# Kernel tuning notes

Measured on AMD Instinct MI355X. Metric: run time of the kernel, lower is better.

Reference implementation:

```python
import jax, jax.numpy as jnp
import numpy as np

B, D = 16384, 1024
H1, H2 = 512, 256
T = 3          # num_tasks
E_SH = 2       # num_shared_experts
E_SP = 2       # num_specific_experts
G = E_SH + E_SP


def setup_inputs() -> dict:
    key = jax.random.key(0)
    ks = jax.random.split(key, 8)
    def glorot(k, shape, fan_in, fan_out):
        return jax.random.normal(k, shape, jnp.float32) * jnp.sqrt(2.0 / (fan_in + fan_out))
    return {
        "x": jax.random.normal(ks[0], (B, D), jnp.float32),
        "shared_W1": glorot(ks[1], (E_SH, D, H1), D, H1),
        "shared_b1": jnp.zeros((E_SH, H1), jnp.float32),
        "shared_W2": glorot(ks[2], (E_SH, H1, H2), H1, H2),
        "shared_b2": jnp.zeros((E_SH, H2), jnp.float32),
        "spec_W1": glorot(ks[3], (T, E_SP, D, H1), D, H1),
        "spec_b1": jnp.zeros((T, E_SP, H1), jnp.float32),
        "spec_W2": glorot(ks[4], (T, E_SP, H1, H2), H1, H2),
        "spec_b2": jnp.zeros((T, E_SP, H2), jnp.float32),
        "gate_W": glorot(ks[5], (T, D, G), D, G),
        "gate_b": jnp.zeros((T, G), jnp.float32),
    }


def reference(x, shared_W1, shared_b1, shared_W2, shared_b2,
              spec_W1, spec_b1, spec_W2, spec_b2, gate_W, gate_b):
    # Shared experts: two-layer MLP with relu, batched over experts. [B, E_SH, H2]
    sh = jax.nn.relu(jnp.einsum('bi,eih->beh', x, shared_W1) + shared_b1)
    sh = jax.nn.relu(jnp.einsum('beh,eho->beo', sh, shared_W2) + shared_b2)
    # Task-specific experts, batched over (task, expert). [B, T, E_SP, H2]
    sp = jax.nn.relu(jnp.einsum('bi,teih->bteh', x, spec_W1) + spec_b1)
    sp = jax.nn.relu(jnp.einsum('bteh,teho->bteo', sp, spec_W2) + spec_b2)
    # Gates: single linear layer per task + softmax over G=E_SH+E_SP experts. [B, T, G]
    gate = jax.nn.softmax(jnp.einsum('bi,tig->btg', x, gate_W) + gate_b, axis=-1)
    # Experts stacked in order: shared first, then specific (matches tf.stack order).
    sh_b = jnp.broadcast_to(sh[:, None], (B, T, E_SH, H2))
    experts = jnp.concatenate([sh_b, sp], axis=2)  # [B, T, G, H2]
    # Gate-weighted sum over the expert axis -> per-task outputs [B, T, H2]
    out = jnp.einsum('btgh,btg->bth', experts, gate)
    return out
```

## Files before the change

### kernel.cpp

```cpp
#include <hip/hip_runtime.h>
#include <hip/hip_bf16.h>
#include <stdint.h>

#define B_SZ 16384
#define D_SZ 1024
#define H1_SZ 512
#define H2_SZ 256
#define T_SZ 3
#define ESH 2
#define NE 8

typedef __bf16 bf16x8 __attribute__((ext_vector_type(8)));
typedef float f32x4 __attribute__((ext_vector_type(4)));
typedef unsigned short u16;
typedef u16 u16x8 __attribute__((ext_vector_type(8)));

__device__ __forceinline__ u16 f2bf(float f) {
  union { float f; uint32_t u; } v; v.f = f;
  uint32_t u = v.u;
  uint32_t r = (u + 0x7FFFu + ((u >> 16) & 1u)) >> 16;
  return (u16)r;
}
__device__ __forceinline__ float bf2f(u16 b) {
  union { uint32_t u; float f; } v; v.u = ((uint32_t)b) << 16;
  return v.f;
}

__device__ __forceinline__ void gload16(const u16* src, u16* dst_lds) {
  __builtin_amdgcn_global_load_lds(
      (const __attribute__((address_space(1))) void*)src,
      (__attribute__((address_space(3))) void*)dst_lds, 16, 0, 0);
}

__global__ __launch_bounds__(256) void cast_f32_to_bf16(
    const float* __restrict__ in, u16* __restrict__ out, int n8) {
  int i = blockIdx.x * blockDim.x + threadIdx.x;
  if (i >= n8) return;
  const float4* p = (const float4*)in + (size_t)i * 2;
  float4 a = p[0], b = p[1];
  u16x8 o;
  o[0] = f2bf(a.x); o[1] = f2bf(a.y); o[2] = f2bf(a.z); o[3] = f2bf(a.w);
  o[4] = f2bf(b.x); o[5] = f2bf(b.y); o[6] = f2bf(b.z); o[7] = f2bf(b.w);
  *((u16x8*)out + i) = o;
}

__global__ __launch_bounds__(256) void transpose_cast(
    const float* __restrict__ src, u16* __restrict__ dst, int K, int N) {
  __shared__ float tile[32][33];
  size_t e = blockIdx.z;
  const float* s = src + e * (size_t)K * N;
  u16* d = dst + e * (size_t)K * N;
  int n0 = blockIdx.x * 32, k0 = blockIdx.y * 32;
  int tx = threadIdx.x, ty = threadIdx.y;
#pragma unroll
  for (int i = ty; i < 32; i += 8)
    tile[i][tx] = s[(size_t)(k0 + i) * N + n0 + tx];
  __syncthreads();
#pragma unroll
  for (int i = ty; i < 32; i += 8)
    d[(size_t)(n0 + i) * K + k0 + tx] = f2bf(tile[tx][i]);
}

__global__ __launch_bounds__(512, 2) void gemm_ring(
    const u16* __restrict__ A, size_t strideAe,
    const u16* __restrict__ Bt,
    const float* __restrict__ bias_sh, const float* __restrict__ bias_sp,
    u16* __restrict__ C, int M, int N, int K, int ntn) {
  __shared__ __align__(16) u16 lds[4 * 16384];
  const int tid = threadIdx.x;
  const int wid = tid >> 6, lane = tid & 63;
  const int fr = lane & 15, fq = lane >> 4;
  const int wr = wid >> 2, wc = wid & 3;

  const int nwg = gridDim.x;
  const int bid = blockIdx.x;
  const int l = (bid & 7) * (nwg >> 3) + (bid >> 3);
  const int e = l & 7;
  const int rest = l >> 3;
  const int ntile = rest % ntn;
  const int mtile = rest / ntn;
  const int m0 = mtile * 256, n0 = ntile * 256;

  const u16* Ae = A + (size_t)e * strideAe;
  const u16* Be = Bt + (size_t)e * (size_t)N * K;
  const int NT = K >> 5;

  const int c0 = tid, c1 = 512 + tid;
  const int ar0 = c0 >> 2, as0 = (c0 & 3) ^ ((ar0 >> 1) & 3);
  const int ar1 = c1 >> 2, as1 = (c1 & 3) ^ ((ar1 >> 1) & 3);
  const u16* pA0 = Ae + (size_t)(m0 + ar0) * K + as0 * 8;
  const u16* pA1 = Ae + (size_t)(m0 + ar1) * K + as1 * 8;
  const u16* pB0 = Be + (size_t)(n0 + ar0) * K + as0 * 8;
  const u16* pB1 = Be + (size_t)(n0 + ar1) * K + as1 * 8;
  const int dst0 = (wid * 64) * 8;
  const int dst1 = (512 + wid * 64) * 8;

  int offA[8], offB[4];
#pragma unroll
  for (int m = 0; m < 8; ++m) {
    int r = wr * 128 + m * 16 + fr;
    offA[m] = r * 32 + ((fq ^ ((r >> 1) & 3)) * 8);
  }
#pragma unroll
  for (int n = 0; n < 4; ++n) {
    int cg = wc * 64 + n * 16 + fr;
    offB[n] = 8192 + cg * 32 + ((fq ^ ((cg >> 1) & 3)) * 8);
  }

  f32x4 acc[8][4] = {};

#define STAGE(t) do { const int sbs = ((t) & 3) * 16384;              \
    gload16(pA0 + (t) * 32, &lds[sbs + dst0]);                        \
    gload16(pA1 + (t) * 32, &lds[sbs + dst1]);                        \
    gload16(pB0 + (t) * 32, &lds[sbs + 8192 + dst0]);                 \
    gload16(pB1 + (t) * 32, &lds[sbs + 8192 + dst1]); } while (0)

  STAGE(0); STAGE(1); STAGE(2);
  asm volatile("s_waitcnt vmcnt(8)");
  __builtin_amdgcn_s_barrier();
  __builtin_amdgcn_sched_barrier(0);

  for (int t = 0; t < NT; ++t) {
    const u16* sl = &lds[(t & 3) * 16384];
    bf16x8 av[8], bv[4];
#pragma unroll
    for (int m = 0; m < 8; ++m) av[m] = *(const bf16x8*)&sl[offA[m]];
#pragma unroll
    for (int n = 0; n < 4; ++n) bv[n] = *(const bf16x8*)&sl[offB[n]];
    if (t + 3 < NT) STAGE(t + 3);
    __builtin_amdgcn_s_setprio(1);
#pragma unroll
    for (int m = 0; m < 8; ++m)
#pragma unroll
      for (int n = 0; n < 4; ++n)
        acc[m][n] = __builtin_amdgcn_mfma_f32_16x16x32_bf16(av[m], bv[n], acc[m][n], 0, 0, 0);
    __builtin_amdgcn_s_setprio(0);
    asm volatile("s_waitcnt vmcnt(8)");
    __builtin_amdgcn_s_barrier();
    __builtin_amdgcn_sched_barrier(0);
  }
#undef STAGE

  const float* bias = (e < ESH) ? (bias_sh + (size_t)e * N)
                                : (bias_sp + (size_t)(e - ESH) * N);
  u16* Ce = C + (size_t)e * (size_t)M * N;
  float bb[4];
#pragma unroll
  for (int n = 0; n < 4; ++n) bb[n] = bias[n0 + wc * 64 + n * 16 + fr];

  const int src = (tid >> 5);
  const int cc = (tid & 31) * 8;
#pragma unroll
  for (int half = 0; half < 2; ++half) {
    if (wr == half) {
#pragma unroll
      for (int m = 0; m < 8; ++m) {
#pragma unroll
        for (int n = 0; n < 4; ++n) {
          const int col = wc * 64 + n * 16 + fr;
          f32x4 a = acc[m][n];
#pragma unroll
          for (int r = 0; r < 4; ++r) {
            float v = a[r] + bb[n];
            v = v > 0.f ? v : 0.f;
            lds[(m * 16 + fq * 4 + r) * 256 + col] = f2bf(v);
          }
        }
      }
    }
    __builtin_amdgcn_s_barrier();
#pragma unroll
    for (int pass = 0; pass < 8; ++pass) {
      const int lr = pass * 16 + src;
      const int gr = m0 + half * 128 + lr;
      u16x8 vv = *(const u16x8*)&lds[lr * 256 + cc];
      *(u16x8*)&Ce[(size_t)gr * N + n0 + cc] = vv;
    }
    __builtin_amdgcn_s_barrier();
  }
}

__global__ __launch_bounds__(256) void gates_kernel(
    const float* __restrict__ x, const float* __restrict__ gW,
    const float* __restrict__ gb, float* __restrict__ gates) {
  __shared__ float gw[12][1024];
  const int tid = threadIdx.x;
  for (int i = tid; i < 12 * 1024; i += 256) {
    int tg = i >> 10, k = i & 1023;
    gw[tg][k] = gW[(size_t)(tg >> 2) * 4096 + (size_t)k * 4 + (tg & 3)];
  }
  __syncthreads();
  const int wid = tid >> 6, lane = tid & 63;
  const size_t b = (size_t)blockIdx.x * 4 + wid;
  const float* xr = x + b * 1024;
  float acc[12] = {};
  for (int kk = 0; kk < 16; ++kk) {
    float xv = xr[kk * 64 + lane];
#pragma unroll
    for (int t = 0; t < 12; ++t) acc[t] += xv * gw[t][kk * 64 + lane];
  }
#pragma unroll
  for (int off = 32; off >= 1; off >>= 1)
#pragma unroll
    for (int t = 0; t < 12; ++t) acc[t] += __shfl_xor(acc[t], off);
  if (lane == 0) {
    float* gr = gates + b * 12;
#pragma unroll
    for (int t = 0; t < 3; ++t) {
      float l0 = acc[t * 4 + 0] + gb[t * 4 + 0];
      float l1 = acc[t * 4 + 1] + gb[t * 4 + 1];
      float l2 = acc[t * 4 + 2] + gb[t * 4 + 2];
      float l3 = acc[t * 4 + 3] + gb[t * 4 + 3];
      float mx = fmaxf(fmaxf(l0, l1), fmaxf(l2, l3));
      float e0 = __expf(l0 - mx), e1 = __expf(l1 - mx);
      float e2 = __expf(l2 - mx), e3 = __expf(l3 - mx);
      float inv = 1.f / (e0 + e1 + e2 + e3);
      gr[t * 4 + 0] = e0 * inv; gr[t * 4 + 1] = e1 * inv;
      gr[t * 4 + 2] = e2 * inv; gr[t * 4 + 3] = e3 * inv;
    }
  }
}

__global__ __launch_bounds__(256) void combine_kernel(
    const u16* __restrict__ y2, const float* __restrict__ gates,
    float* __restrict__ out) {
  const int tid = threadIdx.x;
  const int rb = tid >> 5;
  const int hc = (tid & 31) * 8;
  const size_t b = (size_t)blockIdx.x * 8 + rb;
  const float* g = gates + b * 12;
  float acc0[8] = {}, acc1[8] = {}, acc2[8] = {};
#pragma unroll
  for (int e = 0; e < 8; ++e) {
    u16x8 v = *(const u16x8*)&y2[(size_t)e * B_SZ * H2_SZ + b * H2_SZ + hc];
    float f[8];
#pragma unroll
    for (int i = 0; i < 8; ++i) f[i] = bf2f(v[i]);
    if (e < 2) {
      float g0 = g[0 * 4 + e], g1 = g[1 * 4 + e], g2 = g[2 * 4 + e];
#pragma unroll
      for (int i = 0; i < 8; ++i) {
        acc0[i] += g0 * f[i]; acc1[i] += g1 * f[i]; acc2[i] += g2 * f[i];
      }
    } else {
      const int t = (e - 2) >> 1, gi = 2 + ((e - 2) & 1);
      float gv = g[t * 4 + gi];
      float* acc = (t == 0) ? acc0 : (t == 1) ? acc1 : acc2;
#pragma unroll
      for (int i = 0; i < 8; ++i) acc[i] += gv * f[i];
    }
  }
  float* o = out + b * (3 * 256);
  *(float4*)&o[0 * 256 + hc]     = make_float4(acc0[0], acc0[1], acc0[2], acc0[3]);
  *(float4*)&o[0 * 256 + hc + 4] = make_float4(acc0[4], acc0[5], acc0[6], acc0[7]);
  *(float4*)&o[1 * 256 + hc]     = make_float4(acc1[0], acc1[1], acc1[2], acc1[3]);
  *(float4*)&o[1 * 256 + hc + 4] = make_float4(acc1[4], acc1[5], acc1[6], acc1[7]);
  *(float4*)&o[2 * 256 + hc]     = make_float4(acc2[0], acc2[1], acc2[2], acc2[3]);
  *(float4*)&o[2 * 256 + hc + 4] = make_float4(acc2[4], acc2[5], acc2[6], acc2[7]);
}

extern "C" void kernel_launch(void* const* d_in, const int* in_sizes, int n_in,
                              void* d_out, int out_size, void* d_ws, size_t ws_size,
                              hipStream_t stream) {
  (void)in_sizes; (void)n_in; (void)out_size; (void)ws_size;
  const float* x   = (const float*)d_in[0];
  const float* sW1 = (const float*)d_in[1];
  const float* sb1 = (const float*)d_in[2];
  const float* sW2 = (const float*)d_in[3];
  const float* sb2 = (const float*)d_in[4];
  const float* pW1 = (const float*)d_in[5];
  const float* pb1 = (const float*)d_in[6];
  const float* pW2 = (const float*)d_in[7];
  const float* pb2 = (const float*)d_in[8];
  const float* gW  = (const float*)d_in[9];
  const float* gb  = (const float*)d_in[10];

  uint8_t* ws = (uint8_t*)d_ws;
  u16* xb    = (u16*)(ws);
  u16* w1t   = (u16*)(ws + 33554432);
  u16* w2t   = (u16*)(ws + 41943040);
  u16* y1    = (u16*)(ws + 44040192);
  u16* y2    = (u16*)(ws + 178257920);
  float* gts = (float*)(ws + 245366784);

  cast_f32_to_bf16<<<(B_SZ * D_SZ / 8 + 255) / 256, 256, 0, stream>>>(
      x, xb, B_SZ * D_SZ / 8);

  transpose_cast<<<dim3(512 / 32, 1024 / 32, 2), dim3(32, 8), 0, stream>>>(
      sW1, w1t, 1024, 512);
  transpose_cast<<<dim3(512 / 32, 1024 / 32, 6), dim3(32, 8), 0, stream>>>(
      pW1, w1t + (size_t)2 * 1024 * 512, 1024, 512);
  transpose_cast<<<dim3(256 / 32, 512 / 32, 2), dim3(32, 8), 0, stream>>>(
      sW2, w2t, 512, 256);
  transpose_cast<<<dim3(256 / 32, 512 / 32, 6), dim3(32, 8), 0, stream>>>(
      pW2, w2t + (size_t)2 * 512 * 256, 512, 256);

  gates_kernel<<<B_SZ / 4, 256, 0, stream>>>(x, gW, gb, gts);

  gemm_ring<<<(B_SZ / 256) * (512 / 256) * NE, 512, 0, stream>>>(
      xb, 0, w1t, sb1, pb1, y1, B_SZ, 512, 1024, 512 / 256);

  gemm_ring<<<(B_SZ / 256) * (256 / 256) * NE, 512, 0, stream>>>(
      y1, (size_t)B_SZ * 512, w2t, sb2, pb2, y2, B_SZ, 256, 512, 256 / 256);

  combine_kernel<<<B_SZ / 8, 256, 0, stream>>>(y2, gts, (float*)d_out);
}
```

Measured before the change: 324.1 us.

## Shrink GEMM tile to 128x256 with 4 waves and 3-stage LDS ring

Replaces the 256x256, 8-wave GEMM with a 128x256 tile computed by 4 waves, and changes the LDS pipeline from a 4-deep ring to a 3-deep one with prefetch distance 2. The block-to-tile mapping changes from an XCD-interleaved remap to a direct expert-major order. The epilogue writes the whole tile at once through a padded LDS stride of 264. This doubles the grid size and cuts LDS per block so more blocks fit per CU, at the cost of less B-operand reuse per tile and shallower latency hiding.

```diff
diff --git a/kernel.cpp b/kernel.cpp
--- a/kernel.cpp
+++ b/kernel.cpp
@@ -61,73 +61,83 @@
     d[(size_t)(n0 + i) * K + k0 + tx] = f2bf(tile[tx][i]);
 }
 
-__global__ __launch_bounds__(512, 2) void gemm_ring(
+__global__ __launch_bounds__(256, 2) void gemm_ring3(
     const u16* __restrict__ A, size_t strideAe,
     const u16* __restrict__ Bt,
     const float* __restrict__ bias_sh, const float* __restrict__ bias_sp,
-    u16* __restrict__ C, int M, int N, int K, int ntn) {
-  __shared__ __align__(16) u16 lds[4 * 16384];
+    u16* __restrict__ C, int M, int N, int K, int ntn_sh) {
+  __shared__ __align__(16) u16 lds[3 * 12288];
   const int tid = threadIdx.x;
   const int wid = tid >> 6, lane = tid & 63;
   const int fr = lane & 15, fq = lane >> 4;
-  const int wr = wid >> 2, wc = wid & 3;
-
-  const int nwg = gridDim.x;
+  const int wc = wid;
+
   const int bid = blockIdx.x;
-  const int l = (bid & 7) * (nwg >> 3) + (bid >> 3);
-  const int e = l & 7;
-  const int rest = l >> 3;
-  const int ntile = rest % ntn;
-  const int mtile = rest / ntn;
-  const int m0 = mtile * 256, n0 = ntile * 256;
+  const int e = bid & 7;
+  const int r = bid >> 3;
+  const int mtile = r >> ntn_sh;
+  const int ntile = r & ((1 << ntn_sh) - 1);
+  const int m0 = mtile * 128, n0 = ntile * 256;
 
   const u16* Ae = A + (size_t)e * strideAe;
   const u16* Be = Bt + (size_t)e * (size_t)N * K;
   const int NT = K >> 5;
 
-  const int c0 = tid, c1 = 512 + tid;
-  const int ar0 = c0 >> 2, as0 = (c0 & 3) ^ ((ar0 >> 1) & 3);
-  const int ar1 = c1 >> 2, as1 = (c1 & 3) ^ ((ar1 >> 1) & 3);
-  const u16* pA0 = Ae + (size_t)(m0 + ar0) * K + as0 * 8;
-  const u16* pA1 = Ae + (size_t)(m0 + ar1) * K + as1 * 8;
-  const u16* pB0 = Be + (size_t)(n0 + ar0) * K + as0 * 8;
-  const u16* pB1 = Be + (size_t)(n0 + ar1) * K + as1 * 8;
-  const int dst0 = (wid * 64) * 8;
-  const int dst1 = (512 + wid * 64) * 8;
+  const u16* pA[2];
+  const u16* pB[4];
+#pragma unroll
+  for (int p = 0; p < 2; ++p) {
+    int c = p * 256 + tid, row = c >> 2, sl = (c & 3) ^ ((row >> 1) & 3);
+    pA[p] = Ae + (size_t)(m0 + row) * K + sl * 8;
+  }
+#pragma unroll
+  for (int p = 0; p < 4; ++p) {
+    int c = p * 256 + tid, row = c >> 2, sl = (c & 3) ^ ((row >> 1) & 3);
+    pB[p] = Be + (size_t)(n0 + row) * K + sl * 8;
+  }
+  const int wdst = wid * 512;
 
   int offA[8], offB[4];
 #pragma unroll
   for (int m = 0; m < 8; ++m) {
-    int r = wr * 128 + m * 16 + fr;
-    offA[m] = r * 32 + ((fq ^ ((r >> 1) & 3)) * 8);
+    int rr = m * 16 + fr;
+    offA[m] = rr * 32 + ((fq ^ ((rr >> 1) & 3)) * 8);
   }
 #pragma unroll
   for (int n = 0; n < 4; ++n) {
     int cg = wc * 64 + n * 16 + fr;
-    offB[n] = 8192 + cg * 32 + ((fq ^ ((cg >> 1) & 3)) * 8);
+    offB[n] = 4096 + cg * 32 + ((fq ^ ((cg >> 1) & 3)) * 8);
   }
 
   f32x4 acc[8][4] = {};
 
-#define STAGE(t) do { const int sbs = ((t) & 3) * 16384;              \
-    gload16(pA0 + (t) * 32, &lds[sbs + dst0]);                        \
-    gload16(pA1 + (t) * 32, &lds[sbs + dst1]);                        \
-    gload16(pB0 + (t) * 32, &lds[sbs + 8192 + dst0]);                 \
-    gload16(pB1 + (t) * 32, &lds[sbs + 8192 + dst1]); } while (0)
-
-  STAGE(0); STAGE(1); STAGE(2);
-  asm volatile("s_waitcnt vmcnt(8)");
+#define STAGE(t, sb) do {                                             \
+    gload16(pA[0] + (size_t)(t) * 32, &lds[(sb) + wdst]);             \
+    gload16(pA[1] + (size_t)(t) * 32, &lds[(sb) + 2048 + wdst]);      \
+    gload16(pB[0] + (size_t)(t) * 32, &lds[(sb) + 4096 + wdst]);      \
+    gload16(pB[1] + (size_t)(t) * 32, &lds[(sb) + 6144 + wdst]);      \
+    gload16(pB[2] + (size_t)(t) * 32, &lds[(sb) + 8192 + wdst]);      \
+    gload16(pB[3] + (size_t)(t) * 32, &lds[(sb) + 10240 + wdst]); } while (0)
+
+  STAGE(0, 0);
+  STAGE(1, 12288);
+  asm volatile("s_waitcnt vmcnt(6)");
   __builtin_amdgcn_s_barrier();
   __builtin_amdgcn_sched_barrier(0);
 
+  int sb_cur = 0;
   for (int t = 0; t < NT; ++t) {
-    const u16* sl = &lds[(t & 3) * 16384];
+    const u16* sl = &lds[sb_cur];
     bf16x8 av[8], bv[4];
 #pragma unroll
     for (int m = 0; m < 8; ++m) av[m] = *(const bf16x8*)&sl[offA[m]];
 #pragma unroll
     for (int n = 0; n < 4; ++n) bv[n] = *(const bf16x8*)&sl[offB[n]];
-    if (t + 3 < NT) STAGE(t + 3);
+    if (t + 2 < NT) {
+      int sb_n2 = sb_cur + 2 * 12288;
+      if (sb_n2 >= 36864) sb_n2 -= 36864;
+      STAGE(t + 2, sb_n2);
+    }
     __builtin_amdgcn_s_setprio(1);
 #pragma unroll
     for (int m = 0; m < 8; ++m)
@@ -135,9 +145,12 @@
       for (int n = 0; n < 4; ++n)
         acc[m][n] = __builtin_amdgcn_mfma_f32_16x16x32_bf16(av[m], bv[n], acc[m][n], 0, 0, 0);
     __builtin_amdgcn_s_setprio(0);
-    asm volatile("s_waitcnt vmcnt(8)");
+    if (t + 2 < NT)      asm volatile("s_waitcnt vmcnt(6)");
+    else if (t + 1 < NT) asm volatile("s_waitcnt vmcnt(0)");
     __builtin_amdgcn_s_barrier();
     __builtin_amdgcn_sched_barrier(0);
+    sb_cur += 12288;
+    if (sb_cur >= 36864) sb_cur = 0;
   }
 #undef STAGE
 
@@ -148,35 +161,28 @@
 #pragma unroll
   for (int n = 0; n < 4; ++n) bb[n] = bias[n0 + wc * 64 + n * 16 + fr];
 
-  const int src = (tid >> 5);
-  const int cc = (tid & 31) * 8;
-#pragma unroll
-  for (int half = 0; half < 2; ++half) {
-    if (wr == half) {
-#pragma unroll
-      for (int m = 0; m < 8; ++m) {
-#pragma unroll
-        for (int n = 0; n < 4; ++n) {
-          const int col = wc * 64 + n * 16 + fr;
-          f32x4 a = acc[m][n];
-#pragma unroll
-          for (int r = 0; r < 4; ++r) {
-            float v = a[r] + bb[n];
-            v = v > 0.f ? v : 0.f;
-            lds[(m * 16 + fq * 4 + r) * 256 + col] = f2bf(v);
-          }
-        }
+#pragma unroll
+  for (int m = 0; m < 8; ++m) {
+#pragma unroll
+    for (int n = 0; n < 4; ++n) {
+      const int col = wc * 64 + n * 16 + fr;
+      f32x4 a = acc[m][n];
+#pragma unroll
+      for (int rr = 0; rr < 4; ++rr) {
+        float v = a[rr] + bb[n];
+        v = v > 0.f ? v : 0.f;
+        lds[(m * 16 + fq * 4 + rr) * 264 + col] = f2bf(v);
       }
     }
-    __builtin_amdgcn_s_barrier();
-#pragma unroll
-    for (int pass = 0; pass < 8; ++pass) {
-      const int lr = pass * 16 + src;
-      const int gr = m0 + half * 128 + lr;
-      u16x8 vv = *(const u16x8*)&lds[lr * 256 + cc];
-      *(u16x8*)&Ce[(size_t)gr * N + n0 + cc] = vv;
-    }
-    __builtin_amdgcn_s_barrier();
+  }
+  __builtin_amdgcn_s_barrier();
+  const int cc = (tid & 31) * 8;
+  const int rr8 = tid >> 5;
+#pragma unroll
+  for (int pass = 0; pass < 16; ++pass) {
+    const int lr = pass * 8 + rr8;
+    u16x8 vv = *(const u16x8*)&lds[lr * 264 + cc];
+    *(u16x8*)&Ce[(size_t)(m0 + lr) * N + n0 + cc] = vv;
   }
 }
 
@@ -297,11 +303,11 @@
 
   gates_kernel<<<B_SZ / 4, 256, 0, stream>>>(x, gW, gb, gts);
 
-  gemm_ring<<<(B_SZ / 256) * (512 / 256) * NE, 512, 0, stream>>>(
-      xb, 0, w1t, sb1, pb1, y1, B_SZ, 512, 1024, 512 / 256);
-
-  gemm_ring<<<(B_SZ / 256) * (256 / 256) * NE, 512, 0, stream>>>(
-      y1, (size_t)B_SZ * 512, w2t, sb2, pb2, y2, B_SZ, 256, 512, 256 / 256);
+  gemm_ring3<<<(B_SZ / 128) * (512 / 256) * NE, 256, 0, stream>>>(
+      xb, 0, w1t, sb1, pb1, y1, B_SZ, 512, 1024, 1);
+
+  gemm_ring3<<<(B_SZ / 128) * (256 / 256) * NE, 256, 0, stream>>>(
+      y1, (size_t)B_SZ * 512, w2t, sb2, pb2, y2, B_SZ, 256, 512, 0);
 
   combine_kernel<<<B_SZ / 8, 256, 0, stream>>>(y2, gts, (float*)d_out);
 }
```

Result: faster. 309.1 us (-4.6%).
